# Optimization experiments

Measured on AMD Instinct MI355X. Metric: run time of the kernel, lower is better.

## Reference

```python
import jax, jax.numpy as jnp
import numpy as np

NUM_MOVIES = 100000
MOVIE_FEAT = 128
USER_FEAT = 128
BATCH = 16384
N_NBRS = 50
D0, D1, D2 = 256, 256, 128  # layer_dims


def setup_inputs() -> dict:
    key = jax.random.key(0)
    ks = jax.random.split(key, 16)
    inp = {
        "users": jax.random.normal(ks[0], (BATCH, USER_FEAT), jnp.float32),
        "pos_movies": jax.random.normal(ks[1], (BATCH, MOVIE_FEAT), jnp.float32),
        "neg_movies": jax.random.normal(ks[2], (BATCH, MOVIE_FEAT), jnp.float32),
        "user_ids": jax.random.randint(ks[3], (BATCH,), 0, BATCH),
        "pos_movie_ids": jax.random.randint(ks[4], (BATCH,), 0, NUM_MOVIES),
        "neg_movie_ids": jax.random.randint(ks[5], (BATCH,), 0, NUM_MOVIES),
        "nbr_ids": jax.random.randint(ks[6], (BATCH, N_NBRS), 0, NUM_MOVIES),
        # learned params / buffers
        "movie_table": jax.random.normal(ks[7], (NUM_MOVIES, MOVIE_FEAT), jnp.float32),
        "Wu": jax.random.normal(ks[8], (USER_FEAT, D0), jnp.float32) * (1.0 / np.sqrt(USER_FEAT)),
        "bu": jnp.zeros((D0,), jnp.float32),
        "Wm": jax.random.normal(ks[9], (MOVIE_FEAT, D0), jnp.float32) * (1.0 / np.sqrt(MOVIE_FEAT)),
        "bm": jnp.zeros((D0,), jnp.float32),
        "W1": jax.random.normal(ks[10], (D0, D1), jnp.float32) * (1.0 / np.sqrt(D0)),
        "b1": jnp.zeros((D1,), jnp.float32),
        "W2": jax.random.normal(ks[11], (D1, D2), jnp.float32) * (1.0 / np.sqrt(D1)),
        "b2": jnp.zeros((D2,), jnp.float32),
    }
    return inp


def reference(users, pos_movies, neg_movies, user_ids, pos_movie_ids, neg_movie_ids,
              nbr_ids, movie_table, Wu, bu, Wm, bm, W1, b1, W2, b2):
    # user_projection / movie_projection
    user_emb = users @ Wu + bu                      # [B, D0]
    movie_emb = movie_table @ Wm + bm               # [N, D0]
    pos_emb = movie_emb[pos_movie_ids]              # [B, D0]
    neg_emb = movie_emb[neg_movie_ids]              # [B, D0]
    # vectorized replacement of the per-user neighbor gather + mean loop
    nbr_mean = jnp.mean(movie_emb[nbr_ids], axis=1)  # [B, N_NBRS, D0] -> [B, D0]
    user_emb = user_emb + nbr_mean
    x = jnp.stack([user_emb, pos_emb, neg_emb], axis=0)  # [3, B, D0]
    x = jax.nn.relu(x @ W1 + b1)
    x = jax.nn.relu(x @ W2 + b2)
    return (x[0], x[1], x[2])
```

## Files before the change

### kernel.cpp

```cpp
#include <hip/hip_runtime.h>
#include <hip/hip_bf16.h>

#define BATCH_N   16384
#define FEAT      128
#define NNBR      50
#define NUM_MOVIES_N 100000

typedef short  short8  __attribute__((ext_vector_type(8)));
typedef float  floatx4 __attribute__((ext_vector_type(4)));
typedef unsigned int u32;

__device__ __forceinline__ __hip_bfloat16 f2bf(float x) { return __float2bfloat16(x); }
__device__ __forceinline__ float bfb2f(short s) {
  union { u32 u; float f; } c; c.u = ((u32)(unsigned short)s) << 16; return c.f;
}

__device__ __forceinline__ void gld16(const __hip_bfloat16* g, __hip_bfloat16* l) {
  __builtin_amdgcn_global_load_lds(
      (const __attribute__((address_space(1))) u32*)g,
      (__attribute__((address_space(3))) u32*)l, 16, 0, 0);
}

__device__ __forceinline__ floatx4 mfma16(short8 a, short8 b, floatx4 c) {
  return __builtin_amdgcn_mfma_f32_16x16x32_bf16(a, b, c, 0, 0, 0);
}

#define CONV_BLOCKS (NUM_MOVIES_N * FEAT / (256 * 8))
__global__ __launch_bounds__(256) void prep_all(
    const float* __restrict__ t, __hip_bfloat16* __restrict__ tb,
    const float* __restrict__ Wu, const float* __restrict__ Wm,
    const float* __restrict__ W1, const float* __restrict__ W2,
    const float* __restrict__ bu, const float* __restrict__ bm,
    __hip_bfloat16* __restrict__ WcatT, __hip_bfloat16* __restrict__ WmT,
    __hip_bfloat16* __restrict__ W1T,  __hip_bfloat16* __restrict__ W2T,
    float* __restrict__ bc) {
  int bid = blockIdx.x;
  if (bid < CONV_BLOCKS) {
    size_t i = ((size_t)bid * 256 + threadIdx.x) * 8;
    float4 v0 = *(const float4*)(t + i);
    float4 v1 = *(const float4*)(t + i + 4);
    __hip_bfloat16 o[8];
    o[0] = f2bf(v0.x); o[1] = f2bf(v0.y); o[2] = f2bf(v0.z); o[3] = f2bf(v0.w);
    o[4] = f2bf(v1.x); o[5] = f2bf(v1.y); o[6] = f2bf(v1.z); o[7] = f2bf(v1.w);
    *(short8*)(tb + i) = *(short8*)o;
  } else {
    int idx = (bid - CONV_BLOCKS) * 256 + threadIdx.x;
    int n = idx & 255, k = idx >> 8;
    float v = (k < 128) ? Wu[k * 256 + n] : Wm[(k - 128) * 256 + n];
    WcatT[n * 256 + k] = f2bf(v);
    W1T[n * 256 + k]   = f2bf(W1[k * 256 + n]);
    if (k < 128) WmT[n * 128 + k] = f2bf(Wm[k * 256 + n]);
    if (idx < 32768) {
      int k2 = idx >> 7, n2 = idx & 127;
      W2T[n2 * 256 + k2] = f2bf(W2[k2 * 128 + n2]);
    }
    if (idx < 256) bc[idx] = bu[idx] + bm[idx];
  }
}

__global__ __launch_bounds__(256) void gather_user(
    const float* __restrict__ users, const int* __restrict__ nbr_ids,
    const __hip_bfloat16* __restrict__ tb, __hip_bfloat16* __restrict__ A_user) {
  int row  = (blockIdx.x << 2) + (threadIdx.x >> 6);
  int lane = threadIdx.x & 63;
  int quad = lane >> 4, sl = lane & 15;
  const int* nb = nbr_ids + row * NNBR;
  float acc[8] = {0.f, 0.f, 0.f, 0.f, 0.f, 0.f, 0.f, 0.f};
  #pragma unroll
  for (int it = 0; it < 13; ++it) {
    int j = it * 4 + quad;
    if (j < NNBR) {
      int id = nb[j];
      short8 v = *(const short8*)(tb + (size_t)id * FEAT + sl * 8);
      #pragma unroll
      for (int e = 0; e < 8; ++e) acc[e] += bfb2f(v[e]);
    }
  }
  __hip_bfloat16 o[8];
  #pragma unroll
  for (int e = 0; e < 8; ++e) {
    float v = acc[e];
    v += __shfl_xor(v, 16, 64);
    v += __shfl_xor(v, 32, 64);
    o[e] = f2bf(v * (1.f / NNBR));
  }
  if (quad == 0)
    *(short8*)(A_user + (size_t)row * 256 + 128 + sl * 8) = *(short8*)o;
  float2 uv = ((const float2*)(users + (size_t)row * FEAT))[lane];
  __hip_bfloat162 t0; t0.x = f2bf(uv.x); t0.y = f2bf(uv.y);
  ((__hip_bfloat162*)(A_user + (size_t)row * 256))[lane] = t0;
}

template <int K0, int NCOL, bool RELU, bool TOGLB>
__device__ __forceinline__ void layer(
    const __hip_bfloat16* Ain,
    const __hip_bfloat16* __restrict__ Wt, const float* __restrict__ bias,
    __hip_bfloat16* Olds, float* __restrict__ Oglb,
    int wid, int quad, int lrow) {
  constexpr int KK = K0 / 32;
  constexpr int JN = NCOL / 128;
  const int c0 = wid * JN * 16;

  short8 bfr[JN][KK];
  float  bv[JN];
  #pragma unroll
  for (int j = 0; j < JN; ++j) {
    #pragma unroll
    for (int kc = 0; kc < KK; ++kc)
      bfr[j][kc] = *(const short8*)(Wt + (size_t)(c0 + j * 16 + lrow) * K0 +
                                    kc * 32 + quad * 8);
    bv[j] = bias[c0 + j * 16 + lrow];
  }

  #pragma unroll
  for (int it = 0; it < 4; ++it) {
    int r = it * 16 + lrow;
    short8 af[KK];
    #pragma unroll
    for (int kc = 0; kc < KK; ++kc)
      af[kc] = *(const short8*)&Ain[r * K0 + (((kc * 4 + quad) ^ (r & 7)) << 3)];
    floatx4 pa[JN], pb[JN];
    #pragma unroll
    for (int j = 0; j < JN; ++j) { pa[j] = {}; pb[j] = {}; }
    #pragma unroll
    for (int kc = 0; kc < KK; kc += 2)
      #pragma unroll
      for (int j = 0; j < JN; ++j) {
        pa[j] = mfma16(af[kc],     bfr[j][kc],     pa[j]);
        pb[j] = mfma16(af[kc + 1], bfr[j][kc + 1], pb[j]);
      }
    #pragma unroll
    for (int j = 0; j < JN; ++j) {
      floatx4 a = pa[j] + pb[j];
      int col = c0 + j * 16 + lrow;
      #pragma unroll
      for (int rr = 0; rr < 4; ++rr) {
        int row = it * 16 + quad * 4 + rr;
        float v = a[rr] + bv[j];
        if (RELU) v = fmaxf(v, 0.f);
        if (TOGLB) {
          Oglb[(size_t)row * NCOL + col] = v;
        } else {
          int ch = col >> 3;
          Olds[row * 256 + (((ch ^ (row & 7)) << 3) | (col & 7))] = f2bf(v);
        }
      }
    }
  }
}

__global__ __launch_bounds__(512)
__attribute__((amdgpu_waves_per_eu(2, 2)))
void fused_mlp(
    const __hip_bfloat16* __restrict__ A_user,
    const __hip_bfloat16* __restrict__ tb,
    const int* __restrict__ pos_ids, const int* __restrict__ neg_ids,
    const __hip_bfloat16* __restrict__ WcatT,
    const __hip_bfloat16* __restrict__ WmT,
    const __hip_bfloat16* __restrict__ W1T,
    const __hip_bfloat16* __restrict__ W2T,
    const float* __restrict__ bc, const float* __restrict__ bmv,
    const float* __restrict__ b1, const float* __restrict__ b2,
    float* __restrict__ out) {
  __shared__ __hip_bfloat16 A_lds[64 * 256];
  __shared__ __hip_bfloat16 E_lds[64 * 256];

  const int t    = threadIdx.x;
  const int lane = t & 63, wid = t >> 6;
  const int quad = lane >> 4, lrow = lane & 15;
  const int s    = blockIdx.x % 3;
  const long m0  = (long)(blockIdx.x / 3) * 64;

  if (s == 0) {
    #pragma unroll
    for (int i = 0; i < 4; ++i) {
      int c = t + i * 512;
      int r = c >> 5, sl = c & 31;
      gld16(A_user + ((size_t)(m0 + r) << 8) + ((sl ^ (r & 7)) << 3),
            A_lds + (c << 3));
    }
  } else {
    const int* ids = (s == 1) ? pos_ids : neg_ids;
    #pragma unroll
    for (int i = 0; i < 2; ++i) {
      int c = t + i * 512;
      int r = c >> 4, sl = c & 15;
      int id = ids[m0 + r];
      gld16(tb + ((size_t)id << 7) + ((sl ^ (r & 7)) << 3),
            A_lds + (c << 3));
    }
  }
  __syncthreads();

  if (s == 0)
    layer<256, 256, false, false>(A_lds, WcatT, bc, E_lds, nullptr,
                                  wid, quad, lrow);
  else
    layer<128, 256, false, false>(A_lds, WmT, bmv, E_lds, nullptr,
                                  wid, quad, lrow);
  __syncthreads();

  layer<256, 256, true, false>(E_lds, W1T, b1, A_lds, nullptr,
                               wid, quad, lrow);
  __syncthreads();

  layer<256, 128, true, true>(A_lds, W2T, b2, nullptr,
                              out + ((size_t)s * BATCH_N + m0) * 128,
                              wid, quad, lrow);
}

extern "C" void kernel_launch(void* const* d_in, const int* in_sizes, int n_in,
                              void* d_out, int out_size, void* d_ws, size_t ws_size,
                              hipStream_t stream) {
  const float* users   = (const float*)d_in[0];
  const int*   pos_ids = (const int*)d_in[4];
  const int*   neg_ids = (const int*)d_in[5];
  const int*   nbr_ids = (const int*)d_in[6];
  const float* table   = (const float*)d_in[7];
  const float* Wu = (const float*)d_in[8];
  const float* bu = (const float*)d_in[9];
  const float* Wm = (const float*)d_in[10];
  const float* bm = (const float*)d_in[11];
  const float* W1 = (const float*)d_in[12];
  const float* b1 = (const float*)d_in[13];
  const float* W2 = (const float*)d_in[14];
  const float* b2 = (const float*)d_in[15];
  float* out = (float*)d_out;

  char* p = (char*)d_ws;
  auto carve = [&](size_t bytes) { char* r = p; p += (bytes + 255) & ~(size_t)255; return r; };
  __hip_bfloat16* tb     = (__hip_bfloat16*)carve((size_t)NUM_MOVIES_N * FEAT * 2);
  __hip_bfloat16* WcatT  = (__hip_bfloat16*)carve(256 * 256 * 2);
  __hip_bfloat16* WmT    = (__hip_bfloat16*)carve(256 * 128 * 2);
  __hip_bfloat16* W1T    = (__hip_bfloat16*)carve(256 * 256 * 2);
  __hip_bfloat16* W2T    = (__hip_bfloat16*)carve(128 * 256 * 2);
  float*          bc     = (float*)carve(256 * 4);
  __hip_bfloat16* A_user = (__hip_bfloat16*)carve((size_t)BATCH_N * 256 * 2);

  prep_all<<<CONV_BLOCKS + 256, 256, 0, stream>>>(
      table, tb, Wu, Wm, W1, W2, bu, bm, WcatT, WmT, W1T, W2T, bc);
  gather_user<<<BATCH_N / 4, 256, 0, stream>>>(users, nbr_ids, tb, A_user);
  fused_mlp<<<3 * BATCH_N / 64, 512, 0, stream>>>(
      A_user, tb, pos_ids, neg_ids, WcatT, WmT, W1T, W2T,
      bc, bm, b1, b2, out);
}
```

Baseline: 200.5 us.

## Fuse neighbor gather and user conversion into the MLP kernel

Removes the separate gather_user kernel and the A_user global buffer. The user-stream blocks of fused_mlp now gather and average the 50 neighbor embeddings and convert the user features directly into the swizzled LDS tile. This saves one kernel launch and a global write and read of a 16384x256 bf16 buffer. In exchange, the gather latency now sits inside the MLP blocks, only one third of the blocks do the long gather, and those blocks run at a low occupancy (2 waves per EU), so the load becomes imbalanced and the gather latency is harder to hide.

```diff
diff --git a/kernel.cpp b/kernel.cpp
--- a/kernel.cpp
+++ b/kernel.cpp
@@ -58,39 +58,6 @@
   }
 }
 
-__global__ __launch_bounds__(256) void gather_user(
-    const float* __restrict__ users, const int* __restrict__ nbr_ids,
-    const __hip_bfloat16* __restrict__ tb, __hip_bfloat16* __restrict__ A_user) {
-  int row  = (blockIdx.x << 2) + (threadIdx.x >> 6);
-  int lane = threadIdx.x & 63;
-  int quad = lane >> 4, sl = lane & 15;
-  const int* nb = nbr_ids + row * NNBR;
-  float acc[8] = {0.f, 0.f, 0.f, 0.f, 0.f, 0.f, 0.f, 0.f};
-  #pragma unroll
-  for (int it = 0; it < 13; ++it) {
-    int j = it * 4 + quad;
-    if (j < NNBR) {
-      int id = nb[j];
-      short8 v = *(const short8*)(tb + (size_t)id * FEAT + sl * 8);
-      #pragma unroll
-      for (int e = 0; e < 8; ++e) acc[e] += bfb2f(v[e]);
-    }
-  }
-  __hip_bfloat16 o[8];
-  #pragma unroll
-  for (int e = 0; e < 8; ++e) {
-    float v = acc[e];
-    v += __shfl_xor(v, 16, 64);
-    v += __shfl_xor(v, 32, 64);
-    o[e] = f2bf(v * (1.f / NNBR));
-  }
-  if (quad == 0)
-    *(short8*)(A_user + (size_t)row * 256 + 128 + sl * 8) = *(short8*)o;
-  float2 uv = ((const float2*)(users + (size_t)row * FEAT))[lane];
-  __hip_bfloat162 t0; t0.x = f2bf(uv.x); t0.y = f2bf(uv.y);
-  ((__hip_bfloat162*)(A_user + (size_t)row * 256))[lane] = t0;
-}
-
 template <int K0, int NCOL, bool RELU, bool TOGLB>
 __device__ __forceinline__ void layer(
     const __hip_bfloat16* Ain,
@@ -152,9 +119,10 @@
 __global__ __launch_bounds__(512)
 __attribute__((amdgpu_waves_per_eu(2, 2)))
 void fused_mlp(
-    const __hip_bfloat16* __restrict__ A_user,
+    const float* __restrict__ users,
     const __hip_bfloat16* __restrict__ tb,
     const int* __restrict__ pos_ids, const int* __restrict__ neg_ids,
+    const int* __restrict__ nbr_ids,
     const __hip_bfloat16* __restrict__ WcatT,
     const __hip_bfloat16* __restrict__ WmT,
     const __hip_bfloat16* __restrict__ W1T,
@@ -172,12 +140,37 @@
   const long m0  = (long)(blockIdx.x / 3) * 64;
 
   if (s == 0) {
-    #pragma unroll
-    for (int i = 0; i < 4; ++i) {
-      int c = t + i * 512;
-      int r = c >> 5, sl = c & 31;
-      gld16(A_user + ((size_t)(m0 + r) << 8) + ((sl ^ (r & 7)) << 3),
-            A_lds + (c << 3));
+    for (int rr = 0; rr < 8; ++rr) {
+      const int r = (wid << 3) | rr;
+      const size_t grow = (size_t)(m0 + r);
+      const int* nb = nbr_ids + grow * NNBR;
+      float acc[8] = {0.f, 0.f, 0.f, 0.f, 0.f, 0.f, 0.f, 0.f};
+      #pragma unroll
+      for (int it = 0; it < 13; ++it) {
+        int j = (it << 2) + quad;
+        if (j < NNBR) {
+          int id = nb[j];
+          short8 v = *(const short8*)(tb + (size_t)id * FEAT + (lrow << 3));
+          #pragma unroll
+          for (int e = 0; e < 8; ++e) acc[e] += bfb2f(v[e]);
+        }
+      }
+      __hip_bfloat16 o[8];
+      #pragma unroll
+      for (int e = 0; e < 8; ++e) {
+        float v = acc[e];
+        v += __shfl_xor(v, 16, 64);
+        v += __shfl_xor(v, 32, 64);
+        o[e] = f2bf(v * (1.f / NNBR));
+      }
+      if (quad == 0) {
+        int ch = 16 + lrow;
+        *(short8*)(A_lds + r * 256 + ((ch ^ (r & 7)) << 3)) = *(short8*)o;
+      }
+      float2 uv = ((const float2*)(users + grow * FEAT))[lane];
+      __hip_bfloat162 t0; t0.x = f2bf(uv.x); t0.y = f2bf(uv.y);
+      int col = lane << 1, ch2 = col >> 3;
+      *(__hip_bfloat162*)(A_lds + r * 256 + ((ch2 ^ (r & 7)) << 3) + (col & 7)) = t0;
     }
   } else {
     const int* ids = (s == 1) ? pos_ids : neg_ids;
@@ -235,12 +228,10 @@
   __hip_bfloat16* W1T    = (__hip_bfloat16*)carve(256 * 256 * 2);
   __hip_bfloat16* W2T    = (__hip_bfloat16*)carve(128 * 256 * 2);
   float*          bc     = (float*)carve(256 * 4);
-  __hip_bfloat16* A_user = (__hip_bfloat16*)carve((size_t)BATCH_N * 256 * 2);
 
   prep_all<<<CONV_BLOCKS + 256, 256, 0, stream>>>(
       table, tb, Wu, Wm, W1, W2, bu, bm, WcatT, WmT, W1T, W2T, bc);
-  gather_user<<<BATCH_N / 4, 256, 0, stream>>>(users, nbr_ids, tb, A_user);
   fused_mlp<<<3 * BATCH_N / 64, 512, 0, stream>>>(
-      A_user, tb, pos_ids, neg_ids, WcatT, WmT, W1T, W2T,
+      users, tb, pos_ids, neg_ids, nbr_ids, WcatT, WmT, W1T, W2T,
       bc, bm, b1, b2, out);
 }
```

Measured after the change: 214.3 us. +6.9%, slower.
